# Kernel tuning notes

Measured on AMD Instinct MI355X. Metric: run time of the kernel, lower is better.

Reference implementation:

```python
import jax, jax.numpy as jnp
import numpy as np

N = 8192
IN_DIM = 512
OUT_DIM = 64
ALPHA = 0.2  # leaky relu negative slope
NEG_INF = -9e15


def setup_inputs() -> dict:
    key = jax.random.key(0)
    k1, k2, k3, k4 = jax.random.split(key, 4)
    h = jax.random.normal(k1, (N, IN_DIM), dtype=jnp.float32)
    adj = jax.random.randint(k2, (N, N), 0, 2, dtype=jnp.int32)
    # xavier-uniform-ish scale for params
    W = jax.random.normal(k3, (IN_DIM, OUT_DIM), dtype=jnp.float32) * (1.414 / np.sqrt(IN_DIM))
    a = jax.random.normal(k4, (2 * OUT_DIM, 1), dtype=jnp.float32) * (1.414 / np.sqrt(2 * OUT_DIM))
    return {"h": h, "adj": adj, "W": W, "a": a}


def reference(h, adj, W, a):
    Wh = h @ W                                   # [N, out]
    Wh1 = Wh @ a[:OUT_DIM]                       # [N, 1]
    Wh2 = Wh @ a[OUT_DIM:]                       # [N, 1]
    e = jax.nn.leaky_relu(Wh1 + Wh2.T, negative_slope=ALPHA)  # [N, N]
    att = jnp.where(adj > 0, e, jnp.float32(NEG_INF))
    att = jax.nn.softmax(att, axis=1)            # masked row softmax
    # dropout is identity in eval mode
    h_next = att @ Wh                            # [N, out]
    return jax.nn.elu(h_next)                    # concat=True path
```

## Files before the change

### kernel.cpp

```cpp
#include <hip/hip_runtime.h>
#include <hip/hip_bf16.h>

#define NN 8192
#define IND 512
#define OUTD 64
#define ALPHA_ 0.2f
#define LOG2E 1.4426950408889634f

typedef float f32x4 __attribute__((ext_vector_type(4)));
typedef short s16x8 __attribute__((ext_vector_type(8)));
typedef int   i32x4 __attribute__((ext_vector_type(4)));
typedef unsigned int uint;

static __device__ __forceinline__ short f2bf(float x) {
    __hip_bfloat16 b = __float2bfloat16(x);
    return *reinterpret_cast<short*>(&b);
}
static __device__ __forceinline__ uint fenc(float f) {
    uint u = __float_as_uint(f);
    return (u & 0x80000000u) ? ~u : (u | 0x80000000u);
}
static __device__ __forceinline__ float fdec(uint k) {
    uint u = (k & 0x80000000u) ? (k & 0x7FFFFFFFu) : ~k;
    return __uint_as_float(u);
}

#define GLD_LDS16(g, d) \
    __builtin_amdgcn_global_load_lds((const __attribute__((address_space(1))) int*)(g), \
                                     (__attribute__((address_space(3))) int*)(d), 16, 0, 0)

__global__ __launch_bounds__(256) void k_wh(const float* __restrict__ h,
                                            const float* __restrict__ W,
                                            const float* __restrict__ a,
                                            __hip_bfloat16* __restrict__ whT,
                                            float* __restrict__ Wh1s,
                                            float* __restrict__ Wh2s,
                                            uint* __restrict__ mxk) {
    __shared__ float hs[8 * IND];
    int tid = threadIdx.x;
    const f32x4* h4 = (const f32x4*)(h + (size_t)blockIdx.x * 8 * IND);
    f32x4* hs4 = (f32x4*)hs;
    #pragma unroll
    for (int t = 0; t < 4; ++t) hs4[tid + t * 256] = h4[tid + t * 256];
    __syncthreads();

    int w = tid >> 6, l = tid & 63;
    int g = l >> 4, lc = l & 15;
    int c4 = lc * 4;
    const float* hrow = hs + (w * 2) * IND;
    f32x4 acc0 = {0.f, 0.f, 0.f, 0.f};
    f32x4 acc1 = {0.f, 0.f, 0.f, 0.f};

    #pragma unroll 4
    for (int k0 = 0; k0 < 128; ++k0) {
        int k = k0 * 4 + g;
        f32x4 wv = *(const f32x4*)(W + k * OUTD + c4);
        float h0 = hrow[k];
        float h1 = hrow[IND + k];
        acc0[0] = fmaf(h0, wv[0], acc0[0]);
        acc0[1] = fmaf(h0, wv[1], acc0[1]);
        acc0[2] = fmaf(h0, wv[2], acc0[2]);
        acc0[3] = fmaf(h0, wv[3], acc0[3]);
        acc1[0] = fmaf(h1, wv[0], acc1[0]);
        acc1[1] = fmaf(h1, wv[1], acc1[1]);
        acc1[2] = fmaf(h1, wv[2], acc1[2]);
        acc1[3] = fmaf(h1, wv[3], acc1[3]);
    }

    #pragma unroll
    for (int e = 0; e < 4; ++e) {
        acc0[e] += __shfl_xor(acc0[e], 16, 64);
        acc0[e] += __shfl_xor(acc0[e], 32, 64);
        acc1[e] += __shfl_xor(acc1[e], 16, 64);
        acc1[e] += __shfl_xor(acc1[e], 32, 64);
    }

    int row0 = blockIdx.x * 8 + w * 2;
    if (g == 0) {
        #pragma unroll
        for (int e = 0; e < 4; ++e) {
            whT[(size_t)(c4 + e) * NN + row0]     = __float2bfloat16(acc0[e]);
            whT[(size_t)(c4 + e) * NN + row0 + 1] = __float2bfloat16(acc1[e]);
        }
    }

    float p10 = 0.f, p20 = 0.f, p11 = 0.f, p21 = 0.f;
    #pragma unroll
    for (int e = 0; e < 4; ++e) {
        float a1 = a[c4 + e], a2 = a[OUTD + c4 + e];
        p10 = fmaf(acc0[e], a1, p10);
        p20 = fmaf(acc0[e], a2, p20);
        p11 = fmaf(acc1[e], a1, p11);
        p21 = fmaf(acc1[e], a2, p21);
    }
    #pragma unroll
    for (int off = 1; off < 16; off <<= 1) {
        p10 += __shfl_xor(p10, off, 64);
        p20 += __shfl_xor(p20, off, 64);
        p11 += __shfl_xor(p11, off, 64);
        p21 += __shfl_xor(p21, off, 64);
    }
    if (l == 0) {
        float s20 = p20 * LOG2E, s21 = p21 * LOG2E;
        Wh1s[row0]     = p10 * LOG2E;  Wh2s[row0]     = s20;
        Wh1s[row0 + 1] = p11 * LOG2E;  Wh2s[row0 + 1] = s21;
        atomicMax(mxk, fenc(fmaxf(s20, s21)));
    }
}

__global__ __launch_bounds__(512) void k_gat(const int* __restrict__ adj,
                                             const __hip_bfloat16* __restrict__ whT,
                                             const float* __restrict__ Wh1s,
                                             const float* __restrict__ Wh2s,
                                             const uint* __restrict__ mxk,
                                             float* __restrict__ out) {
    __shared__ char smem[49152];
    int (*sbuf)[16][256] = (int(*)[16][256])smem;
    float (*lacc)[16][65] = (float(*)[16][65])smem;
    float (*lls)[16] = (float(*)[16])(smem + 8 * 16 * 65 * 4);

    int tid = threadIdx.x;
    int w   = tid >> 6;
    int l   = tid & 63;
    int lr  = l & 15;
    int grp = l >> 4;
    int ib  = blockIdx.x * 16;
    int row = ib + lr;

    float wh1s = Wh1s[row];
    float t0 = wh1s + fdec(*mxk);
    float mcs = fmaxf(t0, ALPHA_ * t0);

    f32x4 acc0 = {0.f, 0.f, 0.f, 0.f};
    f32x4 acc1 = acc0, acc2 = acc0, acc3 = acc0, acc4 = acc0;
    s16x8 bones;
    #pragma unroll
    for (int e = 0; e < 8; ++e) bones[e] = (short)0x3F80;

    int r0 = 2 * w, r1 = 2 * w + 1;
    const int* g0 = adj + (size_t)(ib + r0) * NN + ((l * 4 - 8 * r0) & 255);
    const int* g1 = adj + (size_t)(ib + r1) * NN + ((l * 4 - 8 * r1) & 255);

    int w0 = w * 32 + grp * 8;
    int p0 = (w0 + 8 * lr) & 255;
    int p1 = (w0 + 4 + 8 * lr) & 255;

    const __hip_bfloat16* bp = whT + (size_t)lr * NN;

#define STAGE(b, itc) do {                                   \
        GLD_LDS16(g0 + (size_t)(itc) * 256, &sbuf[b][r0][0]); \
        GLD_LDS16(g1 + (size_t)(itc) * 256, &sbuf[b][r1][0]); \
    } while (0)

    STAGE(0, 0);
    STAGE(1, 1);

    for (int it = 0; it < 32; ++it) {
        __syncthreads();
        if (it < 30) STAGE((it + 2) % 3, it + 2);

        const int* rb = &sbuf[it % 3][lr][0];
        i32x4 a0 = *(const i32x4*)(rb + p0);
        i32x4 a1 = *(const i32x4*)(rb + p1);

        int jl = it * 256 + w0;
        f32x4 w20 = *(const f32x4*)(Wh2s + jl);
        f32x4 w21 = *(const f32x4*)(Wh2s + jl + 4);
        s16x8 b0 = *(const s16x8*)(bp + jl);
        s16x8 b1 = *(const s16x8*)(bp + (size_t)16 * NN + jl);
        s16x8 b2 = *(const s16x8*)(bp + (size_t)32 * NN + jl);
        s16x8 b3 = *(const s16x8*)(bp + (size_t)48 * NN + jl);

        s16x8 af;
        #pragma unroll
        for (int e = 0; e < 4; ++e) {
            float t = wh1s + w20[e];
            float x = fmaxf(t, ALPHA_ * t);
            float p = exp2f(x - mcs);
            p = (a0[e] != 0) ? p : 0.f;
            af[e] = f2bf(p);
        }
        #pragma unroll
        for (int e = 0; e < 4; ++e) {
            float t = wh1s + w21[e];
            float x = fmaxf(t, ALPHA_ * t);
            float p = exp2f(x - mcs);
            p = (a1[e] != 0) ? p : 0.f;
            af[e + 4] = f2bf(p);
        }
        acc0 = __builtin_amdgcn_mfma_f32_16x16x32_bf16(af, b0, acc0, 0, 0, 0);
        acc1 = __builtin_amdgcn_mfma_f32_16x16x32_bf16(af, b1, acc1, 0, 0, 0);
        acc2 = __builtin_amdgcn_mfma_f32_16x16x32_bf16(af, b2, acc2, 0, 0, 0);
        acc3 = __builtin_amdgcn_mfma_f32_16x16x32_bf16(af, b3, acc3, 0, 0, 0);
        acc4 = __builtin_amdgcn_mfma_f32_16x16x32_bf16(af, bones, acc4, 0, 0, 0);
    }
#undef STAGE

    __syncthreads();

    #pragma unroll
    for (int reg = 0; reg < 4; ++reg) {
        int rr = grp * 4 + reg;
        lacc[w][rr][lr]      = acc0[reg];
        lacc[w][rr][16 + lr] = acc1[reg];
        lacc[w][rr][32 + lr] = acc2[reg];
        lacc[w][rr][48 + lr] = acc3[reg];
    }
    if (lr == 0) {
        #pragma unroll
        for (int reg = 0; reg < 4; ++reg) lls[w][grp * 4 + reg] = acc4[reg];
    }
    __syncthreads();

    #pragma unroll
    for (int t = 0; t < 2; ++t) {
        int idx = tid + t * 512;
        int rr = idx >> 6, c = idx & 63;
        float v = 0.f, ls = 0.f;
        #pragma unroll
        for (int ww = 0; ww < 8; ++ww) {
            v += lacc[ww][rr][c];
            ls += lls[ww][rr];
        }
        float hv = v / ls;
        out[(size_t)(ib + rr) * OUTD + c] = hv > 0.f ? hv : exp2f(hv * LOG2E) - 1.f;
    }
}

extern "C" void kernel_launch(void* const* d_in, const int* in_sizes, int n_in,
                              void* d_out, int out_size, void* d_ws, size_t ws_size,
                              hipStream_t stream) {
    const float* h   = (const float*)d_in[0];
    const int*   adj = (const int*)d_in[1];
    const float* W   = (const float*)d_in[2];
    const float* a   = (const float*)d_in[3];
    float* out = (float*)d_out;

    char* ws = (char*)d_ws;
    __hip_bfloat16*  whT  = (__hip_bfloat16*)ws;
    float*           Wh1s = (float*)(ws + 1048576);
    float*           Wh2s = Wh1s + NN;
    uint*            mxk  = (uint*)(Wh2s + NN);

    hipMemsetAsync(mxk, 0, 4, stream);
    k_wh<<<NN / 8, 256, 0, stream>>>(h, W, a, whT, Wh1s, Wh2s, mxk);
    k_gat<<<NN / 16, 512, 0, stream>>>(adj, whT, Wh1s, Wh2s, mxk, out);
}
```

Measured before the change: 161.4 us.

## Pack adjacency into bitmask in a separate kernel and prefetch registers in GAT loop

Adds a k_pack kernel that reads the int32 adjacency matrix once and writes a ballot-based bitmask, 64 columns per 64-bit word. The attention kernel then reads this compact mask instead of staging int rows through LDS with async loads and barriers. The main loop now software-pipelines register loads for the next iteration in place of the LDS triple buffer. The 256 MB adjacency read is still paid in full, now in its own kernel with an extra 8 MB write and read. The gain relies on a simpler, barrier-free attention loop, while adding one launch and making the two phases run one after the other instead of overlapped.

```diff
diff --git a/kernel.cpp b/kernel.cpp
--- a/kernel.cpp
+++ b/kernel.cpp
@@ -11,6 +11,8 @@
 typedef short s16x8 __attribute__((ext_vector_type(8)));
 typedef int   i32x4 __attribute__((ext_vector_type(4)));
 typedef unsigned int uint;
+typedef unsigned long long ull;
+typedef ull ullx2 __attribute__((ext_vector_type(2)));
 
 static __device__ __forceinline__ short f2bf(float x) {
     __hip_bfloat16 b = __float2bfloat16(x);
@@ -25,9 +27,34 @@
     return __uint_as_float(u);
 }
 
-#define GLD_LDS16(g, d) \
-    __builtin_amdgcn_global_load_lds((const __attribute__((address_space(1))) int*)(g), \
-                                     (__attribute__((address_space(3))) int*)(d), 16, 0, 0)
+__global__ __launch_bounds__(256) void k_pack(const int* __restrict__ adj,
+                                              ull* __restrict__ mask) {
+    int tid = threadIdx.x;
+    int w = tid >> 6, l = tid & 63;
+    int row = blockIdx.x * 4 + w;
+    const int* ap = adj + (size_t)row * NN + 4 * l;
+    ull* mp = mask + (size_t)row * 128;
+
+    for (int g = 0; g < 4; ++g) {
+        i32x4 v[8];
+        #pragma unroll
+        for (int k = 0; k < 8; ++k)
+            v[k] = *(const i32x4*)(ap + (g * 8 + k) * 256);
+        #pragma unroll
+        for (int k = 0; k < 8; ++k) {
+            ull b0 = __ballot(v[k][0] != 0);
+            ull b1 = __ballot(v[k][1] != 0);
+            ull b2 = __ballot(v[k][2] != 0);
+            ull b3 = __ballot(v[k][3] != 0);
+            if (l == 0) {
+                ullx2 p0; p0[0] = b0; p0[1] = b1;
+                ullx2 p1; p1[0] = b2; p1[1] = b3;
+                *(ullx2*)(mp + (size_t)(g * 8 + k) * 4)     = p0;
+                *(ullx2*)(mp + (size_t)(g * 8 + k) * 4 + 2) = p1;
+            }
+        }
+    }
+}
 
 __global__ __launch_bounds__(256) void k_wh(const float* __restrict__ h,
                                             const float* __restrict__ W,
@@ -108,17 +135,12 @@
     }
 }
 
-__global__ __launch_bounds__(512) void k_gat(const int* __restrict__ adj,
+__global__ __launch_bounds__(512) void k_gat(const ull* __restrict__ mask,
                                              const __hip_bfloat16* __restrict__ whT,
                                              const float* __restrict__ Wh1s,
                                              const float* __restrict__ Wh2s,
                                              const uint* __restrict__ mxk,
                                              float* __restrict__ out) {
-    __shared__ char smem[49152];
-    int (*sbuf)[16][256] = (int(*)[16][256])smem;
-    float (*lacc)[16][65] = (float(*)[16][65])smem;
-    float (*lls)[16] = (float(*)[16])(smem + 8 * 16 * 65 * 4);
-
     int tid = threadIdx.x;
     int w   = tid >> 6;
     int l   = tid & 63;
@@ -137,67 +159,66 @@
     #pragma unroll
     for (int e = 0; e < 8; ++e) bones[e] = (short)0x3F80;
 
-    int r0 = 2 * w, r1 = 2 * w + 1;
-    const int* g0 = adj + (size_t)(ib + r0) * NN + ((l * 4 - 8 * r0) & 255);
-    const int* g1 = adj + (size_t)(ib + r1) * NN + ((l * 4 - 8 * r1) & 255);
-
+    const ull* mrow = mask + (size_t)row * 128;
+    const __hip_bfloat16* bp = whT + (size_t)lr * NN;
     int w0 = w * 32 + grp * 8;
-    int p0 = (w0 + 8 * lr) & 255;
-    int p1 = (w0 + 4 + 8 * lr) & 255;
-
-    const __hip_bfloat16* bp = whT + (size_t)lr * NN;
-
-#define STAGE(b, itc) do {                                   \
-        GLD_LDS16(g0 + (size_t)(itc) * 256, &sbuf[b][r0][0]); \
-        GLD_LDS16(g1 + (size_t)(itc) * 256, &sbuf[b][r1][0]); \
-    } while (0)
-
-    STAGE(0, 0);
-    STAGE(1, 1);
+    int shamt = 8 * w + 2 * grp;
+
+#define LOADJ(IT, M01, M23, W20, W21, B0, B1, B2, B3)          \
+    M01 = *(const ullx2*)(mrow + (IT) * 4);                    \
+    M23 = *(const ullx2*)(mrow + (IT) * 4 + 2);                \
+    {  int jl = (IT) * 256 + w0;                               \
+       W20 = *(const f32x4*)(Wh2s + jl);                       \
+       W21 = *(const f32x4*)(Wh2s + jl + 4);                   \
+       B0  = *(const s16x8*)(bp + jl);                         \
+       B1  = *(const s16x8*)(bp + (size_t)16 * NN + jl);       \
+       B2  = *(const s16x8*)(bp + (size_t)32 * NN + jl);       \
+       B3  = *(const s16x8*)(bp + (size_t)48 * NN + jl);  }
+
+    ullx2 m01, m23;
+    f32x4 w20, w21;
+    s16x8 b0, b1, b2, b3;
+    LOADJ(0, m01, m23, w20, w21, b0, b1, b2, b3)
 
     for (int it = 0; it < 32; ++it) {
-        __syncthreads();
-        if (it < 30) STAGE((it + 2) % 3, it + 2);
-
-        const int* rb = &sbuf[it % 3][lr][0];
-        i32x4 a0 = *(const i32x4*)(rb + p0);
-        i32x4 a1 = *(const i32x4*)(rb + p1);
-
-        int jl = it * 256 + w0;
-        f32x4 w20 = *(const f32x4*)(Wh2s + jl);
-        f32x4 w21 = *(const f32x4*)(Wh2s + jl + 4);
-        s16x8 b0 = *(const s16x8*)(bp + jl);
-        s16x8 b1 = *(const s16x8*)(bp + (size_t)16 * NN + jl);
-        s16x8 b2 = *(const s16x8*)(bp + (size_t)32 * NN + jl);
-        s16x8 b3 = *(const s16x8*)(bp + (size_t)48 * NN + jl);
+        ullx2 nm01, nm23;
+        f32x4 nw20, nw21;
+        s16x8 nb0, nb1, nb2, nb3;
+        if (it < 31) {
+            LOADJ(it + 1, nm01, nm23, nw20, nw21, nb0, nb1, nb2, nb3)
+        }
+
+        uint s0 = (uint)(m01[0] >> shamt);
+        uint s1 = (uint)(m01[1] >> shamt);
+        uint s2 = (uint)(m23[0] >> shamt);
+        uint s3 = (uint)(m23[1] >> shamt);
 
         s16x8 af;
         #pragma unroll
-        for (int e = 0; e < 4; ++e) {
-            float t = wh1s + w20[e];
+        for (int e = 0; e < 8; ++e) {
+            float t = wh1s + ((e < 4) ? w20[e & 3] : w21[e & 3]);
             float x = fmaxf(t, ALPHA_ * t);
             float p = exp2f(x - mcs);
-            p = (a0[e] != 0) ? p : 0.f;
+            uint sb = (e & 3) == 0 ? s0 : (e & 3) == 1 ? s1 : (e & 3) == 2 ? s2 : s3;
+            p = (sb & (1u << (e >> 2))) ? p : 0.f;
             af[e] = f2bf(p);
-        }
-        #pragma unroll
-        for (int e = 0; e < 4; ++e) {
-            float t = wh1s + w21[e];
-            float x = fmaxf(t, ALPHA_ * t);
-            float p = exp2f(x - mcs);
-            p = (a1[e] != 0) ? p : 0.f;
-            af[e + 4] = f2bf(p);
         }
         acc0 = __builtin_amdgcn_mfma_f32_16x16x32_bf16(af, b0, acc0, 0, 0, 0);
         acc1 = __builtin_amdgcn_mfma_f32_16x16x32_bf16(af, b1, acc1, 0, 0, 0);
         acc2 = __builtin_amdgcn_mfma_f32_16x16x32_bf16(af, b2, acc2, 0, 0, 0);
         acc3 = __builtin_amdgcn_mfma_f32_16x16x32_bf16(af, b3, acc3, 0, 0, 0);
         acc4 = __builtin_amdgcn_mfma_f32_16x16x32_bf16(af, bones, acc4, 0, 0, 0);
-    }
-#undef STAGE
-
-    __syncthreads();
-
+
+        if (it < 31) {
+            m01 = nm01; m23 = nm23;
+            w20 = nw20; w21 = nw21;
+            b0 = nb0; b1 = nb1; b2 = nb2; b3 = nb3;
+        }
+    }
+#undef LOADJ
+
+    __shared__ float lacc[8][16][65];
+    __shared__ float lls[8][16];
     #pragma unroll
     for (int reg = 0; reg < 4; ++reg) {
         int rr = grp * 4 + reg;
@@ -237,12 +258,14 @@
     float* out = (float*)d_out;
 
     char* ws = (char*)d_ws;
-    __hip_bfloat16*  whT  = (__hip_bfloat16*)ws;
-    float*           Wh1s = (float*)(ws + 1048576);
+    ull*             mask = (ull*)ws;
+    __hip_bfloat16*  whT  = (__hip_bfloat16*)(ws + 8388608);
+    float*           Wh1s = (float*)(ws + 8388608 + 1048576);
     float*           Wh2s = Wh1s + NN;
     uint*            mxk  = (uint*)(Wh2s + NN);
 
     hipMemsetAsync(mxk, 0, 4, stream);
+    k_pack<<<NN / 4, 256, 0, stream>>>(adj, mask);
     k_wh<<<NN / 8, 256, 0, stream>>>(h, W, a, whT, Wh1s, Wh2s, mxk);
-    k_gat<<<NN / 16, 512, 0, stream>>>(adj, whT, Wh1s, Wh2s, mxk, out);
-}
+    k_gat<<<NN / 16, 512, 0, stream>>>(mask, whT, Wh1s, Wh2s, mxk, out);
+}
```

Result: slower. 211.3 us (+31.0%).

## Compute attention probabilities once per row into shared bf16 tile, overlap with MFMA

Applied to the files above, without the earlier changes.

Reworks k_gat so each wave computes masked exp probabilities for its two rows, once per element. It reads adj directly from global into registers, replacing the async LDS staging of raw int mask data, and writes swizzled bf16 P tiles into double-buffered shared memory. MFMAs then read P from LDS while the next chunk's adj and Wh2 loads and probability math run in the same iteration, separated by sched barriers. The row-sum MFMA against a ones vector is replaced by fp32 register accumulation and a wave shuffle reduction, using the unrounded fp32 probabilities rather than their bf16 values. It also shrinks LDS and requests 4 blocks per CU.

```diff
diff --git a/kernel.cpp b/kernel.cpp
--- a/kernel.cpp
+++ b/kernel.cpp
@@ -24,10 +24,6 @@
     uint u = (k & 0x80000000u) ? (k & 0x7FFFFFFFu) : ~k;
     return __uint_as_float(u);
 }
-
-#define GLD_LDS16(g, d) \
-    __builtin_amdgcn_global_load_lds((const __attribute__((address_space(1))) int*)(g), \
-                                     (__attribute__((address_space(3))) int*)(d), 16, 0, 0)
 
 __global__ __launch_bounds__(256) void k_wh(const float* __restrict__ h,
                                             const float* __restrict__ W,
@@ -108,16 +104,34 @@
     }
 }
 
-__global__ __launch_bounds__(512) void k_gat(const int* __restrict__ adj,
-                                             const __hip_bfloat16* __restrict__ whT,
-                                             const float* __restrict__ Wh1s,
-                                             const float* __restrict__ Wh2s,
-                                             const uint* __restrict__ mxk,
-                                             float* __restrict__ out) {
-    __shared__ char smem[49152];
-    int (*sbuf)[16][256] = (int(*)[16][256])smem;
-    float (*lacc)[16][65] = (float(*)[16][65])smem;
-    float (*lls)[16] = (float(*)[16])(smem + 8 * 16 * 65 * 4);
+#define MFMA_BF16 __builtin_amdgcn_mfma_f32_16x16x32_bf16
+
+#define PCOMP(V0, V1, W0, W1, WH1, MC, LS, POUT) { \
+    _Pragma("unroll") \
+    for (int e = 0; e < 4; ++e) { \
+        float t_ = (WH1) + (W0)[e]; \
+        float x_ = fmaxf(t_, ALPHA_ * t_); \
+        float p_ = exp2f(x_ - (MC)); \
+        p_ = ((V0)[e] != 0) ? p_ : 0.f; \
+        (LS) += p_; (POUT)[e] = f2bf(p_); \
+    } \
+    _Pragma("unroll") \
+    for (int e = 0; e < 4; ++e) { \
+        float t_ = (WH1) + (W1)[e]; \
+        float x_ = fmaxf(t_, ALPHA_ * t_); \
+        float p_ = exp2f(x_ - (MC)); \
+        p_ = ((V1)[e] != 0) ? p_ : 0.f; \
+        (LS) += p_; (POUT)[e + 4] = f2bf(p_); \
+    } }
+
+__global__ __launch_bounds__(512, 4) void k_gat(const int* __restrict__ adj,
+                                                const __hip_bfloat16* __restrict__ whT,
+                                                const float* __restrict__ Wh1s,
+                                                const float* __restrict__ Wh2s,
+                                                const uint* __restrict__ mxk,
+                                                float* __restrict__ out) {
+    __shared__ __align__(16) char smem[33408];
+    __hip_bfloat16 (*P)[16][512] = (__hip_bfloat16 (*)[16][512])smem;
 
     int tid = threadIdx.x;
     int w   = tid >> 6;
@@ -125,79 +139,90 @@
     int lr  = l & 15;
     int grp = l >> 4;
     int ib  = blockIdx.x * 16;
-    int row = ib + lr;
-
-    float wh1s = Wh1s[row];
-    float t0 = wh1s + fdec(*mxk);
-    float mcs = fmaxf(t0, ALPHA_ * t0);
+    int ra  = 2 * w, rb = 2 * w + 1;
+
+    float mxv  = fdec(*mxk);
+    float wh1a = Wh1s[ib + ra];
+    float wh1b = Wh1s[ib + rb];
+    float ta = wh1a + mxv, tb = wh1b + mxv;
+    float mca = fmaxf(ta, ALPHA_ * ta);
+    float mcb = fmaxf(tb, ALPHA_ * tb);
+
+    const int*   apa = adj + (size_t)(ib + ra) * NN + 8 * l;
+    const int*   apb = adj + (size_t)(ib + rb) * NN + 8 * l;
+    const float* wp  = Wh2s + 8 * l;
+
+    float lsa = 0.f, lsb = 0.f;
+    i32x4 va0, va1, vb0, vb1;
+    f32x4 w20, w21;
+    s16x8 pa, pb;
+
+    va0 = *(const i32x4*)(apa);
+    va1 = *(const i32x4*)(apa + 4);
+    vb0 = *(const i32x4*)(apb);
+    vb1 = *(const i32x4*)(apb + 4);
+    w20 = *(const f32x4*)(wp);
+    w21 = *(const f32x4*)(wp + 4);
+    PCOMP(va0, va1, w20, w21, wh1a, mca, lsa, pa)
+    PCOMP(vb0, vb1, w20, w21, wh1b, mcb, lsb, pb)
+    *(s16x8*)&P[0][ra][(l ^ (ra & 7)) << 3] = pa;
+    *(s16x8*)&P[0][rb][(l ^ (rb & 7)) << 3] = pb;
+    __syncthreads();
 
     f32x4 acc0 = {0.f, 0.f, 0.f, 0.f};
-    f32x4 acc1 = acc0, acc2 = acc0, acc3 = acc0, acc4 = acc0;
-    s16x8 bones;
-    #pragma unroll
-    for (int e = 0; e < 8; ++e) bones[e] = (short)0x3F80;
-
-    int r0 = 2 * w, r1 = 2 * w + 1;
-    const int* g0 = adj + (size_t)(ib + r0) * NN + ((l * 4 - 8 * r0) & 255);
-    const int* g1 = adj + (size_t)(ib + r1) * NN + ((l * 4 - 8 * r1) & 255);
-
-    int w0 = w * 32 + grp * 8;
-    int p0 = (w0 + 8 * lr) & 255;
-    int p1 = (w0 + 4 + 8 * lr) & 255;
-
+    f32x4 acc1 = acc0, acc2 = acc0, acc3 = acc0;
     const __hip_bfloat16* bp = whT + (size_t)lr * NN;
 
-#define STAGE(b, itc) do {                                   \
-        GLD_LDS16(g0 + (size_t)(itc) * 256, &sbuf[b][r0][0]); \
-        GLD_LDS16(g1 + (size_t)(itc) * 256, &sbuf[b][r1][0]); \
-    } while (0)
-
-    STAGE(0, 0);
-    STAGE(1, 1);
-
-    for (int it = 0; it < 32; ++it) {
+    for (int c = 0; c < 16; ++c) {
+        int cur = c & 1;
+        s16x8 a0 = *(const s16x8*)&P[cur][lr][((((w << 3)     + grp)) ^ (lr & 7)) << 3];
+        s16x8 a1 = *(const s16x8*)&P[cur][lr][((((w << 3) + 4 + grp)) ^ (lr & 7)) << 3];
+        size_t jb = (size_t)c * 512 + w * 64 + grp * 8;
+        s16x8 b00 = *(const s16x8*)(bp + jb);
+        s16x8 b01 = *(const s16x8*)(bp + (size_t)16 * NN + jb);
+        s16x8 b02 = *(const s16x8*)(bp + (size_t)32 * NN + jb);
+        s16x8 b03 = *(const s16x8*)(bp + (size_t)48 * NN + jb);
+        s16x8 b10 = *(const s16x8*)(bp + jb + 32);
+        s16x8 b11 = *(const s16x8*)(bp + (size_t)16 * NN + jb + 32);
+        s16x8 b12 = *(const s16x8*)(bp + (size_t)32 * NN + jb + 32);
+        s16x8 b13 = *(const s16x8*)(bp + (size_t)48 * NN + jb + 32);
+        if (c < 15) {
+            int off = (c + 1) * 512;
+            va0 = *(const i32x4*)(apa + off);
+            va1 = *(const i32x4*)(apa + off + 4);
+            vb0 = *(const i32x4*)(apb + off);
+            vb1 = *(const i32x4*)(apb + off + 4);
+            w20 = *(const f32x4*)(wp + off);
+            w21 = *(const f32x4*)(wp + off + 4);
+        }
+        __builtin_amdgcn_sched_barrier(0);
+        acc0 = MFMA_BF16(a0, b00, acc0, 0, 0, 0);
+        acc1 = MFMA_BF16(a0, b01, acc1, 0, 0, 0);
+        acc2 = MFMA_BF16(a0, b02, acc2, 0, 0, 0);
+        acc3 = MFMA_BF16(a0, b03, acc3, 0, 0, 0);
+        acc0 = MFMA_BF16(a1, b10, acc0, 0, 0, 0);
+        acc1 = MFMA_BF16(a1, b11, acc1, 0, 0, 0);
+        acc2 = MFMA_BF16(a1, b12, acc2, 0, 0, 0);
+        acc3 = MFMA_BF16(a1, b13, acc3, 0, 0, 0);
+        __builtin_amdgcn_sched_barrier(0);
+        if (c < 15) {
+            PCOMP(va0, va1, w20, w21, wh1a, mca, lsa, pa)
+            PCOMP(vb0, vb1, w20, w21, wh1b, mcb, lsb, pb)
+            int nxt = cur ^ 1;
+            *(s16x8*)&P[nxt][ra][(l ^ (ra & 7)) << 3] = pa;
+            *(s16x8*)&P[nxt][rb][(l ^ (rb & 7)) << 3] = pb;
+        }
         __syncthreads();
-        if (it < 30) STAGE((it + 2) % 3, it + 2);
-
-        const int* rb = &sbuf[it % 3][lr][0];
-        i32x4 a0 = *(const i32x4*)(rb + p0);
-        i32x4 a1 = *(const i32x4*)(rb + p1);
-
-        int jl = it * 256 + w0;
-        f32x4 w20 = *(const f32x4*)(Wh2s + jl);
-        f32x4 w21 = *(const f32x4*)(Wh2s + jl + 4);
-        s16x8 b0 = *(const s16x8*)(bp + jl);
-        s16x8 b1 = *(const s16x8*)(bp + (size_t)16 * NN + jl);
-        s16x8 b2 = *(const s16x8*)(bp + (size_t)32 * NN + jl);
-        s16x8 b3 = *(const s16x8*)(bp + (size_t)48 * NN + jl);
-
-        s16x8 af;
-        #pragma unroll
-        for (int e = 0; e < 4; ++e) {
-            float t = wh1s + w20[e];
-            float x = fmaxf(t, ALPHA_ * t);
-            float p = exp2f(x - mcs);
-            p = (a0[e] != 0) ? p : 0.f;
-            af[e] = f2bf(p);
-        }
-        #pragma unroll
-        for (int e = 0; e < 4; ++e) {
-            float t = wh1s + w21[e];
-            float x = fmaxf(t, ALPHA_ * t);
-            float p = exp2f(x - mcs);
-            p = (a1[e] != 0) ? p : 0.f;
-            af[e + 4] = f2bf(p);
-        }
-        acc0 = __builtin_amdgcn_mfma_f32_16x16x32_bf16(af, b0, acc0, 0, 0, 0);
-        acc1 = __builtin_amdgcn_mfma_f32_16x16x32_bf16(af, b1, acc1, 0, 0, 0);
-        acc2 = __builtin_amdgcn_mfma_f32_16x16x32_bf16(af, b2, acc2, 0, 0, 0);
-        acc3 = __builtin_amdgcn_mfma_f32_16x16x32_bf16(af, b3, acc3, 0, 0, 0);
-        acc4 = __builtin_amdgcn_mfma_f32_16x16x32_bf16(af, bones, acc4, 0, 0, 0);
-    }
-#undef STAGE
-
-    __syncthreads();
-
+    }
+
+    #pragma unroll
+    for (int off = 1; off < 64; off <<= 1) {
+        lsa += __shfl_xor(lsa, off, 64);
+        lsb += __shfl_xor(lsb, off, 64);
+    }
+
+    float (*lacc)[16][65] = (float (*)[16][65])smem;
+    float* lls = (float*)(smem + 33280);
     #pragma unroll
     for (int reg = 0; reg < 4; ++reg) {
         int rr = grp * 4 + reg;
@@ -206,24 +231,18 @@
         lacc[w][rr][32 + lr] = acc2[reg];
         lacc[w][rr][48 + lr] = acc3[reg];
     }
-    if (lr == 0) {
-        #pragma unroll
-        for (int reg = 0; reg < 4; ++reg) lls[w][grp * 4 + reg] = acc4[reg];
-    }
+    if (l == 0) { lls[ra] = lsa; lls[rb] = lsb; }
     __syncthreads();
 
     #pragma unroll
     for (int t = 0; t < 2; ++t) {
         int idx = tid + t * 512;
-        int rr = idx >> 6, c = idx & 63;
-        float v = 0.f, ls = 0.f;
+        int rr = idx >> 6, cc = idx & 63;
+        float v = 0.f;
         #pragma unroll
-        for (int ww = 0; ww < 8; ++ww) {
-            v += lacc[ww][rr][c];
-            ls += lls[ww][rr];
-        }
-        float hv = v / ls;
-        out[(size_t)(ib + rr) * OUTD + c] = hv > 0.f ? hv : exp2f(hv * LOG2E) - 1.f;
+        for (int ww = 0; ww < 8; ++ww) v += lacc[ww][rr][cc];
+        float hv = v / lls[rr];
+        out[(size_t)(ib + rr) * OUTD + cc] = hv > 0.f ? hv : exp2f(hv * LOG2E) - 1.f;
     }
 }
 
```

After: 162.5 us. About the same (+0.7%).
